# Optimization experiments

Measured on AMD Instinct MI355X. Metric: run time of the kernel, lower is better.

## Reference

```python
import jax, jax.numpy as jnp
import numpy as np

EMBED_DIM = 256; NUM_HEADS = 8; NUM_LEVELS = 4; NUM_POINTS = 4; FFN_DIM = 1024
SHAPES = [(128, 128), (64, 64), (32, 32), (16, 16)]
LN_EPS = 1e-5


def setup_inputs() -> dict:
    key = jax.random.key(0)
    ks = jax.random.split(key, 12)
    B = 2; C = EMBED_DIM
    Lin = sum(h * w for h, w in SHAPES)
    starts = np.concatenate([[0], np.cumsum([h * w for h, w in SHAPES])[:-1]])
    MLP2 = NUM_HEADS * NUM_LEVELS * NUM_POINTS
    p = lambda k, *s: jax.random.normal(k, s, jnp.float32) * 0.05
    return {
        "src": jax.random.normal(ks[0], (B, Lin, C), jnp.float32),
        "pos": jax.random.normal(ks[1], (B, Lin, C), jnp.float32),
        "reference_points": jax.random.uniform(ks[2], (B, Lin, NUM_LEVELS, 2), jnp.float32),
        "Wv": p(ks[3], C, C), "bv": jnp.zeros((C,), jnp.float32),
        "Wo": p(ks[4], C, MLP2 * 2),
        "bo": jax.random.uniform(ks[5], (MLP2 * 2,), jnp.float32, -2.0, 2.0),
        "Wa": p(ks[6], C, MLP2), "ba": jnp.zeros((MLP2,), jnp.float32),
        "Wout": p(ks[7], C, C), "bout": jnp.zeros((C,), jnp.float32),
        "gamma": jnp.ones((C,), jnp.float32), "beta": jnp.zeros((C,), jnp.float32),
        "W1": p(ks[8], C, FFN_DIM), "b1": jnp.zeros((FFN_DIM,), jnp.float32),
        "W2": p(ks[9], FFN_DIM, C), "b2": jnp.zeros((C,), jnp.float32),
        "spatial_shapes": jnp.array(SHAPES, dtype=jnp.int32),
        "level_start_index": jnp.array(starts, dtype=jnp.int32),
        "padding_mask": jnp.zeros((B, Lin), dtype=bool),
    }


def _layer_norm(x, g, b):
    m = jnp.mean(x, axis=-1, keepdims=True)
    v = jnp.mean((x - m) ** 2, axis=-1, keepdims=True)
    return (x - m) * jax.lax.rsqrt(v + LN_EPS) * g + b


def _bilinear_sample(val, loc, H, W):
    # val: [B, M, H*W, D]; loc: [B, M, Q, P, 2] normalized [0,1] (x, y)
    # matches torch grid_sample(align_corners=False, padding_mode='zeros')
    x = loc[..., 0] * W - 0.5
    y = loc[..., 1] * H - 0.5
    x0 = jnp.floor(x); y0 = jnp.floor(y)
    lx = x - x0; ly = y - y0
    x0 = x0.astype(jnp.int32); y0 = y0.astype(jnp.int32)
    Bm, M, Q, P = x0.shape
    out = jnp.zeros(val.shape[:2] + (Q, P, val.shape[-1]), val.dtype)
    corners = ((0, 0, (1 - lx) * (1 - ly)), (1, 0, lx * (1 - ly)),
               (0, 1, (1 - lx) * ly), (1, 1, lx * ly))
    for dx, dy, w in corners:
        xi = x0 + dx; yi = y0 + dy
        valid = (xi >= 0) & (xi < W) & (yi >= 0) & (yi < H)
        idx = jnp.clip(yi, 0, H - 1) * W + jnp.clip(xi, 0, W - 1)  # [B,M,Q,P]
        g = jnp.take_along_axis(val, idx.reshape(Bm, M, Q * P, 1), axis=2)
        g = g.reshape(Bm, M, Q, P, -1)
        out = out + (w * valid)[..., None] * g
    return out  # [B, M, Q, P, D]


def _forward(src, pos, reference_points, Wv, bv, Wo, bo, Wa, ba, Wout, bout,
             gamma, beta, W1, b1, W2, b2, spatial_shapes, level_start_index,
             padding_mask):
    M, L, P = NUM_HEADS, NUM_LEVELS, NUM_POINTS
    B, Lin, C = src.shape
    D = C // M
    shapes = np.asarray(spatial_shapes)          # static level geometry
    starts = np.asarray(level_start_index)
    query = src + pos
    value = src @ Wv + bv
    value = jnp.where(padding_mask[..., None], 0.0, value)
    value = value.reshape(B, Lin, M, D).transpose(0, 2, 1, 3)  # [B,M,Lin,D]
    Lq = query.shape[1]
    off = (query @ Wo + bo).reshape(B, Lq, M, L, P, 2)
    attn = jax.nn.softmax((query @ Wa + ba).reshape(B, Lq, M, L * P), axis=-1)
    attn = attn.reshape(B, Lq, M, L, P).transpose(0, 2, 1, 3, 4)  # [B,M,Lq,L,P]
    # offset normalizer is (W, H) per level
    normalizer = jnp.stack([spatial_shapes[:, 1], spatial_shapes[:, 0]], -1).astype(src.dtype)
    loc = reference_points[:, :, None, :, None, :] + off / normalizer[None, None, None, :, None, :]
    loc = loc.transpose(0, 2, 1, 3, 4, 5)  # [B,M,Lq,L,P,2]
    out = jnp.zeros((B, Lq, M, D), src.dtype)
    for l in range(L):
        H, W = int(shapes[l, 0]), int(shapes[l, 1])
        s = int(starts[l])
        vl = value[:, :, s:s + H * W, :]
        samp = _bilinear_sample(vl, loc[:, :, :, l], H, W)  # [B,M,Lq,P,D]
        out = out + jnp.einsum('bmqp,bmqpd->bqmd', attn[:, :, :, l], samp)
    src2 = out.reshape(B, Lq, C) @ Wout + bout
    x = _layer_norm(src + src2, gamma, beta)   # residual + norm (dropout is eval identity)
    h = jax.nn.relu(x @ W1 + b1)               # Mlp, no second residual in this module
    return h @ W2 + b2


def reference(src, pos, reference_points, Wv, bv, Wo, bo, Wa, ba, Wout, bout,
              gamma, beta, W1, b1, W2, b2, spatial_shapes, level_start_index,
              padding_mask):
    return _forward(src, pos, reference_points, Wv, bv, Wo, bo, Wa, ba, Wout,
                    bout, gamma, beta, W1, b1, W2, b2, spatial_shapes,
                    level_start_index, padding_mask)
```

## Files before the change

### kernel.cpp

```cpp
#include <hip/hip_runtime.h>
#include <hip/hip_bf16.h>
#include <math.h>

#define B_SZ   2
#define LIN    21760
#define C_DIM  256
#define M_H    8
#define D_H    32
#define NLEV   4
#define NPTS   4
#define FFN    1024
#define NTOK   (B_SZ * LIN)
#define NTILE  (NTOK / 32)
#define NCONV  (NTOK * C_DIM / 4 / 256)
#define LN_EPS 1e-5f

typedef __bf16 bf16;
typedef bf16  bf16x4 __attribute__((ext_vector_type(4)));
typedef bf16  bf16x8 __attribute__((ext_vector_type(8)));
typedef float f32x4  __attribute__((ext_vector_type(4)));

__device__ __constant__ int c_Ht[4] = {128, 64, 32, 16};
__device__ __constant__ int c_Wt[4] = {128, 64, 32, 16};
__device__ __constant__ int c_St[4] = {0, 16384, 20480, 21504};

static __device__ __forceinline__ float bf2f(unsigned short u) {
    union { float f; unsigned int i; } c;
    c.i = ((unsigned int)u) << 16;
    return c.f;
}

__global__ __launch_bounds__(256) void k_prep(const float* __restrict__ src,
                                              const float* __restrict__ pos,
                                              bf16* __restrict__ srcb,
                                              bf16* __restrict__ qb,
                                              const float* __restrict__ Wv,
                                              const float* __restrict__ Wo,
                                              const float* __restrict__ Wa,
                                              const float* __restrict__ Wout,
                                              const float* __restrict__ W1,
                                              const float* __restrict__ W2,
                                              bf16* __restrict__ Wvt,
                                              bf16* __restrict__ Wqt,
                                              bf16* __restrict__ Woutt,
                                              bf16* __restrict__ W1t,
                                              bf16* __restrict__ W2t) {
    __shared__ float tile[32][33];
    const int bid = blockIdx.x;
    if (bid < NCONV) {
        const int i = bid * 256 + threadIdx.x;
        const float4 s4 = ((const float4*)src)[i];
        const float4 p4 = ((const float4*)pos)[i];
        bf16x4 sb, qb4;
        sb.x = (bf16)s4.x; sb.y = (bf16)s4.y; sb.z = (bf16)s4.z; sb.w = (bf16)s4.w;
        qb4.x = (bf16)(s4.x + p4.x); qb4.y = (bf16)(s4.y + p4.y);
        qb4.z = (bf16)(s4.z + p4.z); qb4.w = (bf16)(s4.w + p4.w);
        ((bf16x4*)srcb)[i] = sb;
        ((bf16x4*)qb)[i]   = qb4;
        return;
    }
    int b = bid - NCONV;
    const float* W; bf16* Wt; int K, N, ntn;
    if      (b < 64)  { W = Wv;   Wt = Wvt;           K = 256;  N = 256;  ntn = 8;            }
    else if (b < 128) { W = Wo;   Wt = Wqt;           K = 256;  N = 256;  ntn = 8;  b -= 64;  }
    else if (b < 160) { W = Wa;   Wt = Wqt + 65536;   K = 256;  N = 128;  ntn = 4;  b -= 128; }
    else if (b < 224) { W = Wout; Wt = Woutt;         K = 256;  N = 256;  ntn = 8;  b -= 160; }
    else if (b < 480) { W = W1;   Wt = W1t;           K = 256;  N = 1024; ntn = 32; b -= 224; }
    else              { W = W2;   Wt = W2t;           K = 1024; N = 256;  ntn = 8;  b -= 480; }

    const int bx = b % ntn;
    const int by = b / ntn;
    const int tx = threadIdx.x & 31, ty = threadIdx.x >> 5;
    const int n0 = bx * 32, k0 = by * 32;
#pragma unroll
    for (int i = 0; i < 32; i += 8)
        tile[ty + i][tx] = W[(long)(k0 + ty + i) * N + n0 + tx];
    __syncthreads();
#pragma unroll
    for (int i = 0; i < 32; i += 8)
        Wt[(long)(n0 + ty + i) * K + k0 + tx] = (bf16)tile[tx][ty + i];
}

#define GEMM_PROLOG(Aptr, BID)                                                \
    const int t = threadIdx.x;                                                \
    const int lane = t & 63, w = t >> 6;                                      \
    const int c0 = lane & 15, kg = lane >> 4;                                 \
    const long tok0 = (long)(BID) * 32;                                       \
    {                                                                         \
        const bf16x8* src8 = (const bf16x8*)((Aptr) + tok0 * C_DIM);          \
        bf16x8* dst8 = (bf16x8*)xs;                                           \
        for (int i = t; i < 1024; i += 256)                                   \
            dst8[i ^ ((i >> 5) & 7)] = src8[i];                               \
    }                                                                         \
    __syncthreads();                                                          \
    bf16x8 afr[2][8];                                                         \
    _Pragma("unroll")                                                         \
    for (int mh = 0; mh < 2; ++mh) {                                          \
        const int m = mh * 16 + c0;                                           \
        _Pragma("unroll")                                                     \
        for (int kc = 0; kc < 8; ++kc) {                                      \
            const int chunk = m * 32 + kc * 4 + kg;                           \
            afr[mh][kc] = ((const bf16x8*)xs)[chunk ^ (m & 7)];               \
        }                                                                     \
    }

__global__ __launch_bounds__(256) void k_vq(const bf16* __restrict__ srcb,
                                            const bf16* __restrict__ qbuf,
                                            const bf16* __restrict__ Wvt,
                                            const float* __restrict__ bv,
                                            bf16* __restrict__ value,
                                            const bf16* __restrict__ Wqt,
                                            const float* __restrict__ bo,
                                            const float* __restrict__ ba,
                                            const float* __restrict__ refp,
                                            float* __restrict__ loc,
                                            float* __restrict__ att) {
    __shared__ bf16 xs[32 * 256];
    if (blockIdx.x < NTILE) {
        GEMM_PROLOG(srcb, blockIdx.x)

        const int b = (int)(tok0 / LIN);
        const int qbase = (int)(tok0 - (long)b * LIN);

#pragma unroll
        for (int nt = 0; nt < 4; ++nt) {
            const int n = w * 64 + nt * 16 + c0;
            f32x4 a0 = {0.f, 0.f, 0.f, 0.f};
            f32x4 a1 = {0.f, 0.f, 0.f, 0.f};
            const bf16* wrow = Wvt + (long)n * 256 + kg * 8;
#pragma unroll
            for (int kc = 0; kc < 8; ++kc) {
                const bf16x8 bfr = *(const bf16x8*)(wrow + kc * 32);
                a0 = __builtin_amdgcn_mfma_f32_16x16x32_bf16(afr[0][kc], bfr, a0, 0, 0, 0);
                a1 = __builtin_amdgcn_mfma_f32_16x16x32_bf16(afr[1][kc], bfr, a1, 0, 0, 0);
            }
            const float bb = bv[n];
            const int m = n >> 5, d = n & 31;
            bf16* vb = value + ((long)(b * M_H + m) * LIN) * D_H + d;
#pragma unroll
            for (int r = 0; r < 4; ++r) {
                const int q0 = qbase + kg * 4 + r;
                vb[(long)q0 * D_H]        = (bf16)(a0[r] + bb);
                vb[(long)(q0 + 16) * D_H] = (bf16)(a1[r] + bb);
            }
        }
    } else {
        GEMM_PROLOG(qbuf, blockIdx.x - NTILE)

#pragma unroll
        for (int nt = 0; nt < 6; ++nt) {
            const int n = w * 96 + nt * 16 + c0;
            f32x4 a0 = {0.f, 0.f, 0.f, 0.f};
            f32x4 a1 = {0.f, 0.f, 0.f, 0.f};
            const bf16* wrow = Wqt + (long)n * 256 + kg * 8;
#pragma unroll
            for (int kc = 0; kc < 8; ++kc) {
                const bf16x8 bfr = *(const bf16x8*)(wrow + kc * 32);
                a0 = __builtin_amdgcn_mfma_f32_16x16x32_bf16(afr[0][kc], bfr, a0, 0, 0, 0);
                a1 = __builtin_amdgcn_mfma_f32_16x16x32_bf16(afr[1][kc], bfr, a1, 0, 0, 0);
            }
            if (n < 256) {
                const int l = (n >> 3) & 3;
                const int c = n & 1;
                const float rnorm = 1.f / ((c == 0) ? (float)c_Wt[l] : (float)c_Ht[l]);
                const float bb = bo[n];
#pragma unroll
                for (int r = 0; r < 4; ++r) {
                    const long t0 = tok0 + kg * 4 + r;
                    const long t1 = t0 + 16;
                    loc[t0 * C_DIM + n] = refp[t0 * 8 + l * 2 + c] + (a0[r] + bb) * rnorm;
                    loc[t1 * C_DIM + n] = refp[t1 * 8 + l * 2 + c] + (a1[r] + bb) * rnorm;
                }
            } else {
                const int j = n - 256;
                const float bb = ba[j];
#pragma unroll
                for (int r = 0; r < 4; ++r) {
                    const long t0 = tok0 + kg * 4 + r;
                    att[t0 * 128 + j]        = a0[r] + bb;
                    att[(t0 + 16) * 128 + j] = a1[r] + bb;
                }
            }
        }
    }
}

__global__ __launch_bounds__(256) void k_samp(const unsigned short* __restrict__ value,
                                              const float* __restrict__ loc,
                                              const float* __restrict__ att,
                                              bf16* __restrict__ outb) {
    __shared__ int4   soff[128];
    __shared__ float4 swgt[128];
    const int t = threadIdx.x;
    const long tok = blockIdx.x;

    if (t < 128) {
        const float lg = att[tok * 128 + t];
        float mx = lg;
#pragma unroll
        for (int s = 1; s < 16; s <<= 1) mx = fmaxf(mx, __shfl_xor(mx, s));
        const float e = expf(lg - mx);
        float sm = e;
#pragma unroll
        for (int s = 1; s < 16; s <<= 1) sm += __shfl_xor(sm, s);
        const float a = e / sm;

        const float2 xy = ((const float2*)loc)[tok * 128 + t];
        const int l = (t >> 2) & 3;
        const int H = c_Ht[l], W = c_Wt[l], s0 = c_St[l];
        const float x = fmaf(xy.x, (float)W, -0.5f);
        const float y = fmaf(xy.y, (float)H, -0.5f);
        const float x0f = floorf(x), y0f = floorf(y);
        const float fx = x - x0f, fy = y - y0f;
        const int x0 = (int)x0f, y0 = (int)y0f;

        const int xi0 = min(max(x0, 0), W - 1);
        const int xi1 = min(max(x0 + 1, 0), W - 1);
        const int yi0 = min(max(y0, 0), H - 1);
        const int yi1 = min(max(y0 + 1, 0), H - 1);
        const float mx0 = (x0 >= 0 && x0 < W) ? 1.f : 0.f;
        const float mx1 = (x0 + 1 < W)        ? 1.f : 0.f;
        const float my0 = (y0 >= 0 && y0 < H) ? 1.f : 0.f;
        const float my1 = (y0 + 1 < H)        ? 1.f : 0.f;
        const float gx0 = (1.f - fx) * mx0, gx1 = fx * ((x0 + 1 >= 0) ? mx1 : 0.f);
        const float gy0 = (1.f - fy) * my0, gy1 = fy * ((y0 + 1 >= 0) ? my1 : 0.f);

        const int r0 = (s0 + yi0 * W) * D_H;
        const int r1 = (s0 + yi1 * W) * D_H;
        soff[t] = (int4){r0 + xi0 * D_H, r0 + xi1 * D_H, r1 + xi0 * D_H, r1 + xi1 * D_H};
        swgt[t] = (float4){a * gx0 * gy0, a * gx1 * gy0, a * gx0 * gy1, a * gx1 * gy1};
    }
    __syncthreads();

    const int m = t >> 5, d = t & 31;
    const int b = (int)(tok / LIN);
    const unsigned short* vb = value + ((long)(b * M_H + m)) * LIN * D_H + d;

    float acc = 0.f;
#pragma unroll
    for (int p = 0; p < 16; ++p) {
        const int jj = m * 16 + p;
        const int4   o = soff[jj];
        const float4 wv = swgt[jj];
        acc = fmaf(bf2f(vb[o.x]), wv.x, acc);
        acc = fmaf(bf2f(vb[o.y]), wv.y, acc);
        acc = fmaf(bf2f(vb[o.z]), wv.z, acc);
        acc = fmaf(bf2f(vb[o.w]), wv.w, acc);
    }
    outb[tok * C_DIM + t] = (bf16)acc;
}

__global__ __launch_bounds__(256) void k_post_mfma(const bf16* __restrict__ A,
                                                   const bf16* __restrict__ Bw,
                                                   const float* __restrict__ bout,
                                                   const float* __restrict__ src,
                                                   const float* __restrict__ g_,
                                                   const float* __restrict__ be_,
                                                   bf16* __restrict__ xb) {
    __shared__ bf16 xs[32 * 256];
    __shared__ float yt[32][256];
    GEMM_PROLOG(A, blockIdx.x)

#pragma unroll
    for (int nt = 0; nt < 4; ++nt) {
        const int n = w * 64 + nt * 16 + c0;
        f32x4 a0 = {0.f, 0.f, 0.f, 0.f};
        f32x4 a1 = {0.f, 0.f, 0.f, 0.f};
        const bf16* wrow = Bw + (long)n * 256 + kg * 8;
#pragma unroll
        for (int kc = 0; kc < 8; ++kc) {
            const bf16x8 bfr = *(const bf16x8*)(wrow + kc * 32);
            a0 = __builtin_amdgcn_mfma_f32_16x16x32_bf16(afr[0][kc], bfr, a0, 0, 0, 0);
            a1 = __builtin_amdgcn_mfma_f32_16x16x32_bf16(afr[1][kc], bfr, a1, 0, 0, 0);
        }
        const float bb = bout[n];
#pragma unroll
        for (int r = 0; r < 4; ++r) {
            const int row = kg * 4 + r;
            yt[row][n]      = a0[r] + bb + src[(tok0 + row) * C_DIM + n];
            yt[row + 16][n] = a1[r] + bb + src[(tok0 + row + 16) * C_DIM + n];
        }
    }
    __syncthreads();

    const float4 g4 = ((const float4*)g_)[lane];
    const float4 b4 = ((const float4*)be_)[lane];
#pragma unroll
    for (int rr = 0; rr < 8; ++rr) {
        const int row = w * 8 + rr;
        const float4 y4 = *(const float4*)&yt[row][lane * 4];
        float s1 = y4.x + y4.y + y4.z + y4.w;
        float s2 = y4.x * y4.x + y4.y * y4.y + y4.z * y4.z + y4.w * y4.w;
#pragma unroll
        for (int s = 1; s < 64; s <<= 1) {
            s1 += __shfl_xor(s1, s);
            s2 += __shfl_xor(s2, s);
        }
        const float mean = s1 * (1.f / 256.f);
        const float var  = s2 * (1.f / 256.f) - mean * mean;
        const float inv  = rsqrtf(var + LN_EPS);
        bf16x4 o;
        o.x = (bf16)((y4.x - mean) * inv * g4.x + b4.x);
        o.y = (bf16)((y4.y - mean) * inv * g4.y + b4.y);
        o.z = (bf16)((y4.z - mean) * inv * g4.z + b4.z);
        o.w = (bf16)((y4.w - mean) * inv * g4.w + b4.w);
        *(bf16x4*)(xb + (tok0 + row) * C_DIM + lane * 4) = o;
    }
}

__global__ __launch_bounds__(256) void k_ffn_mfma(const bf16* __restrict__ x,
                                                  const bf16* __restrict__ W1t,
                                                  const float* __restrict__ b1,
                                                  const bf16* __restrict__ W2t,
                                                  const float* __restrict__ b2,
                                                  float* __restrict__ out) {
    __shared__ bf16 hs0[32 * 256];
    __shared__ bf16 hs1[32 * 256];
    const int lane = threadIdx.x & 63, w = threadIdx.x >> 6;
    const int c0 = lane & 15, kg = lane >> 4;
    const long tok0 = (long)blockIdx.x * 32;

    bf16x8 afr[2][8];
#pragma unroll
    for (int mh = 0; mh < 2; ++mh) {
        const bf16* arow = x + (tok0 + mh * 16 + c0) * C_DIM + kg * 8;
#pragma unroll
        for (int kc = 0; kc < 8; ++kc)
            afr[mh][kc] = *(const bf16x8*)(arow + kc * 32);
    }

    f32x4 acc[2][4];
#pragma unroll
    for (int mh = 0; mh < 2; ++mh)
#pragma unroll
        for (int nt = 0; nt < 4; ++nt)
            acc[mh][nt] = (f32x4){0.f, 0.f, 0.f, 0.f};

#define PHASE_A(cc, hb)                                                       \
    {                                                                         \
        _Pragma("unroll")                                                     \
        for (int nt = 0; nt < 4; ++nt) {                                      \
            const int nl = w * 64 + nt * 16 + c0;                             \
            const int n  = (cc) * 256 + nl;                                   \
            f32x4 a0 = {0.f, 0.f, 0.f, 0.f};                                  \
            f32x4 a1 = {0.f, 0.f, 0.f, 0.f};                                  \
            const bf16* wrow = W1t + (long)n * 256 + kg * 8;                  \
            _Pragma("unroll")                                                 \
            for (int kc = 0; kc < 8; ++kc) {                                  \
                const bf16x8 bfr = *(const bf16x8*)(wrow + kc * 32);          \
                a0 = __builtin_amdgcn_mfma_f32_16x16x32_bf16(afr[0][kc], bfr, a0, 0, 0, 0); \
                a1 = __builtin_amdgcn_mfma_f32_16x16x32_bf16(afr[1][kc], bfr, a1, 0, 0, 0); \
            }                                                                 \
            const float bb = b1[n];                                           \
            _Pragma("unroll")                                                 \
            for (int r = 0; r < 4; ++r) {                                     \
                const int row0 = kg * 4 + r;                                  \
                (hb)[(row0 * 256 + nl)        ^ ((row0 & 7) << 3)] = (bf16)fmaxf(a0[r] + bb, 0.f); \
                (hb)[((row0 + 16) * 256 + nl) ^ ((row0 & 7) << 3)] = (bf16)fmaxf(a1[r] + bb, 0.f); \
            }                                                                 \
        }                                                                     \
    }

#define PHASE_B(cc, hb)                                                       \
    {                                                                         \
        _Pragma("unroll")                                                     \
        for (int kc2 = 0; kc2 < 8; ++kc2) {                                   \
            const int kl = kc2 * 32 + kg * 8;                                 \
            const bf16x8 a0 = *(const bf16x8*)&(hb)[(c0 * 256 + kl)        ^ ((c0 & 7) << 3)]; \
            const bf16x8 a1 = *(const bf16x8*)&(hb)[((c0 + 16) * 256 + kl) ^ ((c0 & 7) << 3)]; \
            _Pragma("unroll")                                                 \
            for (int nt = 0; nt < 4; ++nt) {                                  \
                const int n = w * 64 + nt * 16 + c0;                          \
                const bf16x8 bfr = *(const bf16x8*)(W2t + (long)n * FFN + (cc) * 256 + kl); \
                acc[0][nt] = __builtin_amdgcn_mfma_f32_16x16x32_bf16(a0, bfr, acc[0][nt], 0, 0, 0); \
                acc[1][nt] = __builtin_amdgcn_mfma_f32_16x16x32_bf16(a1, bfr, acc[1][nt], 0, 0, 0); \
            }                                                                 \
        }                                                                     \
    }

    PHASE_A(0, hs0);
    __syncthreads();
    PHASE_B(0, hs0); PHASE_A(1, hs1);
    __syncthreads();
    PHASE_B(1, hs1); PHASE_A(2, hs0);
    __syncthreads();
    PHASE_B(2, hs0); PHASE_A(3, hs1);
    __syncthreads();
    PHASE_B(3, hs1);

#pragma unroll
    for (int nt = 0; nt < 4; ++nt) {
        const int n = w * 64 + nt * 16 + c0;
        const float bb = b2[n];
#pragma unroll
        for (int r = 0; r < 4; ++r) {
            out[(tok0 + kg * 4 + r) * C_DIM + n]      = acc[0][nt][r] + bb;
            out[(tok0 + 16 + kg * 4 + r) * C_DIM + n] = acc[1][nt][r] + bb;
        }
    }
#undef PHASE_A
#undef PHASE_B
}

extern "C" void kernel_launch(void* const* d_in, const int* in_sizes, int n_in,
                              void* d_out, int out_size, void* d_ws, size_t ws_size,
                              hipStream_t stream) {
    const float* src   = (const float*)d_in[0];
    const float* pos   = (const float*)d_in[1];
    const float* refp  = (const float*)d_in[2];
    const float* Wv    = (const float*)d_in[3];
    const float* bv    = (const float*)d_in[4];
    const float* Wo    = (const float*)d_in[5];
    const float* bo    = (const float*)d_in[6];
    const float* Wa    = (const float*)d_in[7];
    const float* ba    = (const float*)d_in[8];
    const float* Wout  = (const float*)d_in[9];
    const float* bout  = (const float*)d_in[10];
    const float* gamma = (const float*)d_in[11];
    const float* beta  = (const float*)d_in[12];
    const float* W1    = (const float*)d_in[13];
    const float* b1    = (const float*)d_in[14];
    const float* W2    = (const float*)d_in[15];
    const float* b2    = (const float*)d_in[16];

    const size_t N256 = (size_t)NTOK * C_DIM;
    bf16*  srcb = (bf16*)d_ws;
    bf16*  qb   = srcb + N256;
    bf16*  val  = qb + N256;
    float* loc  = (float*)(val + N256);
    float* att  = loc + N256;
    bf16*  Wvt  = (bf16*)(att + (size_t)NTOK * 128);
    bf16*  Wqt  = Wvt + 256 * 256;
    bf16*  Woutt= Wqt + 384 * 256;
    bf16*  W1t  = Woutt + 256 * 256;
    bf16*  W2t  = W1t + (size_t)FFN * C_DIM;
    bf16*  outb = srcb;
    bf16*  xb   = qb;

    dim3 blk(256);
    k_prep<<<NCONV + 736, blk, 0, stream>>>(src, pos, srcb, qb,
                                            Wv, Wo, Wa, Wout, W1, W2,
                                            Wvt, Wqt, Woutt, W1t, W2t);
    k_vq  <<<2 * NTILE, blk, 0, stream>>>(srcb, qb, Wvt, bv, val,
                                          Wqt, bo, ba, refp, loc, att);
    k_samp<<<NTOK, blk, 0, stream>>>((const unsigned short*)val, loc, att, outb);
    k_post_mfma<<<NTILE, blk, 0, stream>>>(outb, Woutt, bout, src, gamma, beta, xb);
    k_ffn_mfma <<<NTILE, blk, 0, stream>>>(xb, W1t, b1, W2t, b2, (float*)d_out);
}
```

Measured before the change: 431.6 us.

## Double FFN token tile to 64 rows to halve weight reloads per token

The fused FFN kernel now processes 64 tokens per block instead of 32. Each W1/W2 weight fragment loaded from global memory feeds four MFMA row-tiles instead of two, which halves weight traffic per token. The double-buffered shared hidden tile is replaced by a single 64x256 buffer with an extra barrier per chunk, so the overlap of phase A and phase B is lost. Register use rises from the larger afr/acc arrays, launch bounds now ask for 2 blocks per SM, and the grid is halved.

```diff
diff --git a/kernel.cpp b/kernel.cpp
--- a/kernel.cpp
+++ b/kernel.cpp
@@ -308,98 +308,94 @@
     }
 }
 
-__global__ __launch_bounds__(256) void k_ffn_mfma(const bf16* __restrict__ x,
-                                                  const bf16* __restrict__ W1t,
-                                                  const float* __restrict__ b1,
-                                                  const bf16* __restrict__ W2t,
-                                                  const float* __restrict__ b2,
-                                                  float* __restrict__ out) {
-    __shared__ bf16 hs0[32 * 256];
-    __shared__ bf16 hs1[32 * 256];
+__global__ __launch_bounds__(256, 2) void k_ffn_mfma(const bf16* __restrict__ x,
+                                                     const bf16* __restrict__ W1t,
+                                                     const float* __restrict__ b1,
+                                                     const bf16* __restrict__ W2t,
+                                                     const float* __restrict__ b2,
+                                                     float* __restrict__ out) {
+    __shared__ bf16 hs[64 * 256];
     const int lane = threadIdx.x & 63, w = threadIdx.x >> 6;
     const int c0 = lane & 15, kg = lane >> 4;
-    const long tok0 = (long)blockIdx.x * 32;
-
-    bf16x8 afr[2][8];
-#pragma unroll
-    for (int mh = 0; mh < 2; ++mh) {
+    const long tok0 = (long)blockIdx.x * 64;
+
+    bf16x8 afr[4][8];
+#pragma unroll
+    for (int mh = 0; mh < 4; ++mh) {
         const bf16* arow = x + (tok0 + mh * 16 + c0) * C_DIM + kg * 8;
 #pragma unroll
         for (int kc = 0; kc < 8; ++kc)
             afr[mh][kc] = *(const bf16x8*)(arow + kc * 32);
     }
 
-    f32x4 acc[2][4];
-#pragma unroll
-    for (int mh = 0; mh < 2; ++mh)
+    f32x4 acc[4][4];
+#pragma unroll
+    for (int mh = 0; mh < 4; ++mh)
 #pragma unroll
         for (int nt = 0; nt < 4; ++nt)
             acc[mh][nt] = (f32x4){0.f, 0.f, 0.f, 0.f};
 
-#define PHASE_A(cc, hb)                                                       \
-    {                                                                         \
-        _Pragma("unroll")                                                     \
-        for (int nt = 0; nt < 4; ++nt) {                                      \
-            const int nl = w * 64 + nt * 16 + c0;                             \
-            const int n  = (cc) * 256 + nl;                                   \
-            f32x4 a0 = {0.f, 0.f, 0.f, 0.f};                                  \
-            f32x4 a1 = {0.f, 0.f, 0.f, 0.f};                                  \
-            const bf16* wrow = W1t + (long)n * 256 + kg * 8;                  \
-            _Pragma("unroll")                                                 \
-            for (int kc = 0; kc < 8; ++kc) {                                  \
-                const bf16x8 bfr = *(const bf16x8*)(wrow + kc * 32);          \
-                a0 = __builtin_amdgcn_mfma_f32_16x16x32_bf16(afr[0][kc], bfr, a0, 0, 0, 0); \
-                a1 = __builtin_amdgcn_mfma_f32_16x16x32_bf16(afr[1][kc], bfr, a1, 0, 0, 0); \
-            }                                                                 \
-            const float bb = b1[n];                                           \
-            _Pragma("unroll")                                                 \
-            for (int r = 0; r < 4; ++r) {                                     \
-                const int row0 = kg * 4 + r;                                  \
-                (hb)[(row0 * 256 + nl)        ^ ((row0 & 7) << 3)] = (bf16)fmaxf(a0[r] + bb, 0.f); \
-                (hb)[((row0 + 16) * 256 + nl) ^ ((row0 & 7) << 3)] = (bf16)fmaxf(a1[r] + bb, 0.f); \
-            }                                                                 \
-        }                                                                     \
-    }
-
-#define PHASE_B(cc, hb)                                                       \
-    {                                                                         \
-        _Pragma("unroll")                                                     \
-        for (int kc2 = 0; kc2 < 8; ++kc2) {                                   \
-            const int kl = kc2 * 32 + kg * 8;                                 \
-            const bf16x8 a0 = *(const bf16x8*)&(hb)[(c0 * 256 + kl)        ^ ((c0 & 7) << 3)]; \
-            const bf16x8 a1 = *(const bf16x8*)&(hb)[((c0 + 16) * 256 + kl) ^ ((c0 & 7) << 3)]; \
-            _Pragma("unroll")                                                 \
-            for (int nt = 0; nt < 4; ++nt) {                                  \
-                const int n = w * 64 + nt * 16 + c0;                          \
-                const bf16x8 bfr = *(const bf16x8*)(W2t + (long)n * FFN + (cc) * 256 + kl); \
-                acc[0][nt] = __builtin_amdgcn_mfma_f32_16x16x32_bf16(a0, bfr, acc[0][nt], 0, 0, 0); \
-                acc[1][nt] = __builtin_amdgcn_mfma_f32_16x16x32_bf16(a1, bfr, acc[1][nt], 0, 0, 0); \
-            }                                                                 \
-        }                                                                     \
-    }
-
-    PHASE_A(0, hs0);
-    __syncthreads();
-    PHASE_B(0, hs0); PHASE_A(1, hs1);
-    __syncthreads();
-    PHASE_B(1, hs1); PHASE_A(2, hs0);
-    __syncthreads();
-    PHASE_B(2, hs0); PHASE_A(3, hs1);
-    __syncthreads();
-    PHASE_B(3, hs1);
+    for (int c = 0; c < 4; ++c) {
+        if (c) __syncthreads();
+
+#pragma unroll
+        for (int nt = 0; nt < 4; ++nt) {
+            const int nl = w * 64 + nt * 16 + c0;
+            const int n  = c * 256 + nl;
+            f32x4 a[4];
+#pragma unroll
+            for (int mh = 0; mh < 4; ++mh) a[mh] = (f32x4){0.f, 0.f, 0.f, 0.f};
+            const bf16* wrow = W1t + (long)n * 256 + kg * 8;
+#pragma unroll
+            for (int kc = 0; kc < 8; ++kc) {
+                const bf16x8 bfr = *(const bf16x8*)(wrow + kc * 32);
+#pragma unroll
+                for (int mh = 0; mh < 4; ++mh)
+                    a[mh] = __builtin_amdgcn_mfma_f32_16x16x32_bf16(afr[mh][kc], bfr, a[mh], 0, 0, 0);
+            }
+            const float bb = b1[n];
+#pragma unroll
+            for (int mh = 0; mh < 4; ++mh) {
+#pragma unroll
+                for (int r = 0; r < 4; ++r) {
+                    const int row = mh * 16 + kg * 4 + r;
+                    hs[(row * 256 + nl) ^ ((row & 7) << 3)] = (bf16)fmaxf(a[mh][r] + bb, 0.f);
+                }
+            }
+        }
+        __syncthreads();
+
+#pragma unroll
+        for (int kc2 = 0; kc2 < 8; ++kc2) {
+            const int kl = kc2 * 32 + kg * 8;
+            bf16x8 ah[4];
+#pragma unroll
+            for (int mh = 0; mh < 4; ++mh) {
+                const int row = mh * 16 + c0;
+                ah[mh] = *(const bf16x8*)&hs[(row * 256 + kl) ^ ((row & 7) << 3)];
+            }
+#pragma unroll
+            for (int nt = 0; nt < 4; ++nt) {
+                const int n = w * 64 + nt * 16 + c0;
+                const bf16x8 bfr = *(const bf16x8*)(W2t + (long)n * FFN + c * 256 + kl);
+#pragma unroll
+                for (int mh = 0; mh < 4; ++mh)
+                    acc[mh][nt] = __builtin_amdgcn_mfma_f32_16x16x32_bf16(ah[mh], bfr, acc[mh][nt], 0, 0, 0);
+            }
+        }
+    }
 
 #pragma unroll
     for (int nt = 0; nt < 4; ++nt) {
         const int n = w * 64 + nt * 16 + c0;
         const float bb = b2[n];
 #pragma unroll
-        for (int r = 0; r < 4; ++r) {
-            out[(tok0 + kg * 4 + r) * C_DIM + n]      = acc[0][nt][r] + bb;
-            out[(tok0 + 16 + kg * 4 + r) * C_DIM + n] = acc[1][nt][r] + bb;
-        }
-    }
-#undef PHASE_A
-#undef PHASE_B
+        for (int mh = 0; mh < 4; ++mh) {
+#pragma unroll
+            for (int r = 0; r < 4; ++r)
+                out[(tok0 + mh * 16 + kg * 4 + r) * C_DIM + n] = acc[mh][nt][r] + bb;
+        }
+    }
 }
 
 extern "C" void kernel_launch(void* const* d_in, const int* in_sizes, int n_in,
@@ -445,5 +441,5 @@
                                           Wqt, bo, ba, refp, loc, att);
     k_samp<<<NTOK, blk, 0, stream>>>((const unsigned short*)val, loc, att, outb);
     k_post_mfma<<<NTILE, blk, 0, stream>>>(outb, Woutt, bout, src, gamma, beta, xb);
-    k_ffn_mfma <<<NTILE, blk, 0, stream>>>(xb, W1t, b1, W2t, b2, (float*)d_out);
-}
+    k_ffn_mfma <<<NTOK / 64, blk, 0, stream>>>(xb, W1t, b1, W2t, b2, (float*)d_out);
+}
```

New measurement: 493.6 us. +14.4%, slower.
